# Performance work log

Measured on AMD Instinct MI355X. Metric: run time of the kernel, lower is better.

## Reference

```python
import jax, jax.numpy as jnp
import numpy as np

B, H, N, D = 2, 16, 2048, 64

def setup_inputs() -> dict:
    key = jax.random.key(0)
    ks = jax.random.split(key, 5)
    q = jax.random.normal(ks[0], (B, H, N, D), dtype=jnp.float32)
    k = jax.random.normal(ks[1], (B, H, N, D), dtype=jnp.float32)
    v = jax.random.normal(ks[2], (B, H, N, D), dtype=jnp.float32)
    # 1x1 Conv2d(heads, heads, bias=False) == HxH linear mixing over the head dim
    W_pre = jax.random.normal(ks[3], (H, H), dtype=jnp.float32) * (1.0 / jnp.sqrt(H))
    W_post = jax.random.normal(ks[4], (H, H), dtype=jnp.float32) * (1.0 / jnp.sqrt(H))
    return {"q": q, "k": k, "v": v, "W_pre": W_pre, "W_post": W_post}

def reference(q, k, v, W_pre, W_post):
    heads = q.shape[1]
    d_head = q.shape[-1]
    # original: scale = (1/sqrt(heads)) / sqrt(d_head)
    scale = 1.0 / (jnp.sqrt(jnp.float32(heads)) * jnp.sqrt(jnp.float32(d_head)))
    # pre-softmax talking heads applied to BOTH q and k (head-mixing linear)
    q = jnp.einsum('ef,bfnd->bend', W_pre, q)
    k = jnp.einsum('ef,bfnd->bend', W_pre, k)
    attn_weights = jnp.einsum('bhid,bhjd->bhij', q, k) * scale  # [B,H,N,N]
    i = q.shape[-2]
    j = k.shape[-2]
    causal_mask = jnp.triu(jnp.ones((i, j), dtype=bool), k=1)
    attn_weights = jnp.where(causal_mask, -jnp.inf, attn_weights)
    # softmax computed in float32 (dtype=torch.float32 in attn_fn)
    attn_probs = jax.nn.softmax(attn_weights.astype(jnp.float32), axis=-1)
    # dropout p=0.0 -> identity
    attn_probs = jnp.einsum('ef,bfij->beij', W_post, attn_probs)
    attn_output = jnp.einsum('bhij,bhjd->bhid', attn_probs, v)
    return attn_output
```

## Files before the change

kernel.cpp:

```cpp
#include <hip/hip_runtime.h>
#include <math.h>

typedef _Float16 Hh;
typedef __attribute__((ext_vector_type(8))) _Float16 half8;
typedef __attribute__((ext_vector_type(4))) _Float16 half4;
typedef __attribute__((ext_vector_type(4))) float float4v;

#define B_ 2
#define H_ 16
#define N_ 2048
#define D_ 64
#define ND_ (N_*D_)
#define C1 0.04508422f

#define BAR() asm volatile("s_waitcnt lgkmcnt(0)\n\ts_barrier" ::: "memory")

#define EB_JS 324
#define EB_IS 20
#define PM_ES 580
#define PM_IS 36

__global__ __launch_bounds__(256) void prep_kernel(const float* __restrict__ q,
    const float* __restrict__ k, const float* __restrict__ v,
    const float* __restrict__ Wpre,
    Hh* __restrict__ qb, Hh* __restrict__ kb, Hh* __restrict__ vt2,
    float4* __restrict__ out4, float4* __restrict__ lacc4)
{
    int tid = threadIdx.x;
    int bid = blockIdx.x;
    if (bid < 512) {
        __shared__ float wsh[256];
        wsh[tid] = Wpre[tid];
        __syncthreads();
        int tensor = bid >> 8;
        int g = ((bid & 255) << 8) | tid;
        int b = g >> 15;
        int r = g & 32767;
        const float4* src = (const float4*)(tensor ? k : q);
        Hh* dst = tensor ? kb : qb;
        float4 x[16];
        #pragma unroll
        for (int f=0; f<16; f++) x[f] = src[(size_t)(b*16+f)*32768 + r];
        #pragma unroll
        for (int e=0; e<16; e++) {
            float4 a = make_float4(0.f,0.f,0.f,0.f);
            #pragma unroll
            for (int f=0; f<16; f++) {
                float wv = wsh[e*16+f];
                a.x += wv*x[f].x; a.y += wv*x[f].y; a.z += wv*x[f].z; a.w += wv*x[f].w;
            }
            half4 hv; hv[0]=(Hh)a.x; hv[1]=(Hh)a.y; hv[2]=(Hh)a.z; hv[3]=(Hh)a.w;
            *(half4*)(dst + (size_t)(b*16+e)*ND_ + (size_t)r*4) = hv;
        }
    } else if (bid < 768) {
        __shared__ Hh tile[64*48];
        int tb = bid - 512;
        int be = tb >> 3;
        int jtg = tb & 7;
        const float4* v4 = (const float4*)v;
        for (int u=0; u<8; u++) {
            int jt = jtg*8 + u;
            #pragma unroll
            for (int p=0; p<2; p++) {
                int j = p*16 + (tid>>4);
                int d4 = tid & 15;
                float4 val = v4[(size_t)be*32768 + (size_t)(jt*32+j)*16 + d4];
                tile[(d4*4+0)*48 + j] = (Hh)val.x;
                tile[(d4*4+1)*48 + j] = (Hh)val.y;
                tile[(d4*4+2)*48 + j] = (Hh)val.z;
                tile[(d4*4+3)*48 + j] = (Hh)val.w;
            }
            BAR();
            {
                int d = tid >> 2;
                int jc = (tid & 3) * 8;
                half8 o;
                #pragma unroll
                for (int z=0; z<8; z++) o[z] = tile[d*48 + jc + z];
                *(half8*)(vt2 + ((size_t)(be*64) + jt)*2048 + (size_t)tid*8) = o;
            }
            BAR();
        }
    } else {
        int zid = (bid - 768) * 256 + tid;
        float4 zz = make_float4(0.f,0.f,0.f,0.f);
        #pragma unroll
        for (int u=0; u<4; u++) out4[(size_t)u*262144 + zid] = zz;
        if (zid < 16384) lacc4[zid] = zz;
    }
}

__global__ __launch_bounds__(1024,4) void denom_kernel(const Hh* __restrict__ qb,
    const Hh* __restrict__ kb, float* __restrict__ lacc_g)
{
    int bid = blockIdx.x;
    int s = bid & 7;
    int idx = bid >> 3;
    int b = idx & 1;
    int pr = idx >> 1;
    int tid = threadIdx.x;
    int lane = tid & 63, w = tid >> 6;
    int qd = lane >> 4, c = lane & 15;

    const Hh* qh = qb + (size_t)(b*16 + w)*ND_;
    const Hh* kh = kb + (size_t)(b*16 + w)*ND_;

    for (int half = 0; half < 2; half++) {
        int it = half ? (31 - pr) : pr;
        int i0 = it * 64;

        half8 aq[4][2];
        #pragma unroll
        for (int ig=0; ig<4; ig++) {
            const Hh* qr = qh + (size_t)(i0 + ig*16 + c)*64 + qd*8;
            aq[ig][0] = *(const half8*)qr;
            aq[ig][1] = *(const half8*)(qr+32);
        }
        float lacc[4][4];
        #pragma unroll
        for (int ig=0; ig<4; ig++)
            #pragma unroll
            for (int r=0; r<4; r++) lacc[ig][r] = 0.f;

        int jtmax = 2*it + 1;
        for (int jt = s; jt <= jtmax; jt += 8) {
            int j0 = jt*32;
            #pragma unroll
            for (int jh=0; jh<2; jh++) {
                const Hh* kr = kh + (size_t)(j0 + jh*16 + c)*64 + qd*8;
                half8 b0 = *(const half8*)kr;
                half8 b1 = *(const half8*)(kr+32);
                int j = j0 + jh*16 + c;
                #pragma unroll
                for (int ig=0; ig<4; ig++) {
                    float4v sv = {0.f,0.f,0.f,0.f};
                    sv = __builtin_amdgcn_mfma_f32_16x16x32_f16(aq[ig][0], b0, sv, 0,0,0);
                    sv = __builtin_amdgcn_mfma_f32_16x16x32_f16(aq[ig][1], b1, sv, 0,0,0);
                    #pragma unroll
                    for (int r=0; r<4; r++) {
                        int i = i0 + ig*16 + qd*4 + r;
                        float ev = (j <= i) ? __builtin_amdgcn_exp2f(sv[r]*C1) : 0.f;
                        lacc[ig][r] += ev;
                    }
                }
            }
        }
        #pragma unroll
        for (int ig=0; ig<4; ig++) {
            #pragma unroll
            for (int r=0; r<4; r++) {
                float vs = lacc[ig][r];
                vs += __shfl_xor(vs, 1);
                vs += __shfl_xor(vs, 2);
                vs += __shfl_xor(vs, 4);
                vs += __shfl_xor(vs, 8);
                if (c == 0)
                    unsafeAtomicAdd(&lacc_g[(size_t)(b*16+w)*N_ + i0 + ig*16 + qd*4 + r], vs);
            }
        }
    }
}

__global__ __launch_bounds__(512,4) void attend_kernel(const Hh* __restrict__ qb,
    const Hh* __restrict__ kb, const Hh* __restrict__ vt2,
    const float* __restrict__ lacc_g, const float* __restrict__ Wpost,
    float* __restrict__ out)
{
    __shared__ Hh Ebuf[32*EB_JS];
    __shared__ Hh Pm[16*PM_ES];

    int bid = blockIdx.x;
    int s = (bid & 7) >> 1;
    int idxp = ((bid >> 3) << 1) | (bid & 1);
    int idx = 255 - idxp;
    int b = idx & 1, it = idx >> 1;
    int jtmax = it >> 1;
    if (s > jtmax) return;
    int i0 = it * 16;

    int tid = threadIdx.x;
    int lane = tid & 63, w = tid >> 6;
    int qd = lane >> 4, c = lane & 15;

    int fg = w & 3, jh = w >> 2;
    half8 aq[4][2];
    float lgr[4][4];
    #pragma unroll
    for (int ff=0; ff<4; ff++) {
        int f = 4*fg + ff;
        const Hh* qr = qb + (size_t)((b*16+f)*N_ + i0 + c)*64 + qd*8;
        aq[ff][0] = *(const half8*)qr;
        aq[ff][1] = *(const half8*)(qr+32);
        #pragma unroll
        for (int r=0; r<4; r++)
            lgr[ff][r] = __builtin_amdgcn_logf(
                lacc_g[(size_t)(b*16+f)*N_ + i0 + qd*4 + r]);
    }
    int jh2 = w & 1, ib = 4*(w>>1);
    half4 wf;
    #pragma unroll
    for (int z=0; z<4; z++) wf[z] = (Hh)Wpost[c*16 + qd*4 + z];

    float4v acc[2][4];
    #pragma unroll
    for (int el=0; el<2; el++) for (int nc=0; nc<4; nc++)
        acc[el][nc] = (float4v){0.f,0.f,0.f,0.f};

    auto scores = [&](int jt) {
        int jc = jt*32 + jh*16;
        float4v sv[4];
        #pragma unroll
        for (int ff=0; ff<4; ff++) {
            int f = 4*fg + ff;
            const Hh* kr = kb + (size_t)((b*16+f)*N_ + jc + c)*64 + qd*8;
            half8 b0 = *(const half8*)kr;
            half8 b1 = *(const half8*)(kr+32);
            float4v t = {0.f,0.f,0.f,0.f};
            t = __builtin_amdgcn_mfma_f32_16x16x32_f16(aq[ff][0], b0, t, 0,0,0);
            t = __builtin_amdgcn_mfma_f32_16x16x32_f16(aq[ff][1], b1, t, 0,0,0);
            sv[ff] = t;
        }
        int j = jc + c;
        #pragma unroll
        for (int r=0; r<4; r++) {
            int i = i0 + qd*4 + r;
            half4 h;
            #pragma unroll
            for (int ff=0; ff<4; ff++)
                h[ff] = (Hh)((j <= i) ? __builtin_amdgcn_exp2f(sv[ff][r]*C1 - lgr[ff][r]) : 0.f);
            *(half4*)&Ebuf[(jh*16+c)*EB_JS + (qd*4+r)*EB_IS + fg*4] = h;
        }
    };

    scores(s);
    BAR();

    for (int jt = s; jt <= jtmax; jt += 4) {
        #pragma unroll
        for (int ii=0; ii<4; ii++) {
            int i = ib + ii;
            half4 ef = *(const half4*)&Ebuf[(jh2*16+c)*EB_JS + i*EB_IS + qd*4];
            float4v cc = {0.f,0.f,0.f,0.f};
            cc = __builtin_amdgcn_mfma_f32_16x16x16f16(ef, wf, cc, 0,0,0);
            half4 hv;
            #pragma unroll
            for (int r=0; r<4; r++) hv[r] = (Hh)cc[r];
            *(half4*)&Pm[c*PM_ES + i*PM_IS + jh2*16 + qd*4] = hv;
        }
        BAR();
        #pragma unroll
        for (int el=0; el<2; el++) {
            int e = 2*w + el;
            half8 pa = *(const half8*)&Pm[e*PM_ES + c*PM_IS + qd*8];
            #pragma unroll
            for (int nc=0; nc<4; nc++) {
                const Hh* vr = vt2 + (size_t)((b*16+e)*64 + jt)*2048 + (nc*16+c)*32 + qd*8;
                half8 vb = *(const half8*)vr;
                acc[el][nc] = __builtin_amdgcn_mfma_f32_16x16x32_f16(pa, vb, acc[el][nc], 0,0,0);
            }
        }
        if (jt + 4 <= jtmax) scores(jt + 4);
        BAR();
    }

    #pragma unroll
    for (int el=0; el<2; el++) {
        int e = 2*w + el;
        #pragma unroll
        for (int nc0=0; nc0<4; nc0++) {
            int nc = (nc0 + s) & 3;
            #pragma unroll
            for (int r=0; r<4; r++)
                unsafeAtomicAdd(&out[(size_t)((b*16+e)*N_ + i0 + qd*4 + r)*64 + nc*16 + c],
                                acc[el][nc][r]);
        }
    }
}

extern "C" void kernel_launch(void* const* d_in, const int* in_sizes, int n_in,
                              void* d_out, int out_size, void* d_ws, size_t ws_size,
                              hipStream_t stream) {
    const float* q     = (const float*)d_in[0];
    const float* k     = (const float*)d_in[1];
    const float* v     = (const float*)d_in[2];
    const float* Wpre  = (const float*)d_in[3];
    const float* Wpost = (const float*)d_in[4];
    float* out = (float*)d_out;

    size_t tsz = (size_t)B_*H_*N_*D_;
    Hh* qb = (Hh*)d_ws;
    Hh* kb = qb + tsz;
    Hh* vt2 = kb + tsz;
    float* lacc = (float*)(vt2 + tsz);

    prep_kernel<<<1792, 256, 0, stream>>>(q, k, v, Wpre, qb, kb, vt2,
                                          (float4*)out, (float4*)lacc);
    denom_kernel<<<256, 1024, 0, stream>>>(qb, kb, lacc);
    attend_kernel<<<1024, 512, 0, stream>>>(qb, kb, vt2, lacc, Wpost, out);
}
```

Before: 249.0 us.

## Double attend query tile to 32 rows and pair light/heavy causal tiles per block

The attend kernel now processes 32-row query tiles with 1024-thread blocks. Each K and V load is shared by twice as many query rows, and the LDS score and probability buffers are widened to match. Each block handles two tiles, pr and 63-pr, back to back so the causal work per block is even, and the grid shrinks from 1024 to 256 blocks. The cost is fewer, larger blocks: roughly one block per CU with bigger LDS use, which may reduce latency hiding.

```diff
diff --git a/kernel.cpp b/kernel.cpp
--- a/kernel.cpp
+++ b/kernel.cpp
@@ -15,9 +15,9 @@
 
 #define BAR() asm volatile("s_waitcnt lgkmcnt(0)\n\ts_barrier" ::: "memory")
 
-#define EB_JS 324
+#define EB_JS 644
 #define EB_IS 20
-#define PM_ES 580
+#define PM_ES 1156
 #define PM_IS 36
 
 __global__ __launch_bounds__(256) void prep_kernel(const float* __restrict__ q,
@@ -161,7 +161,7 @@
     }
 }
 
-__global__ __launch_bounds__(512,4) void attend_kernel(const Hh* __restrict__ qb,
+__global__ __launch_bounds__(1024,4) void attend_kernel(const Hh* __restrict__ qb,
     const Hh* __restrict__ kb, const Hh* __restrict__ vt2,
     const float* __restrict__ lacc_g, const float* __restrict__ Wpost,
     float* __restrict__ out)
@@ -171,108 +171,109 @@
 
     int bid = blockIdx.x;
     int s = (bid & 7) >> 1;
-    int idxp = ((bid >> 3) << 1) | (bid & 1);
-    int idx = 255 - idxp;
-    int b = idx & 1, it = idx >> 1;
-    int jtmax = it >> 1;
-    if (s > jtmax) return;
-    int i0 = it * 16;
+    int idx = ((bid >> 3) << 1) | (bid & 1);
+    int b = idx & 1, pr = idx >> 1;
 
     int tid = threadIdx.x;
     int lane = tid & 63, w = tid >> 6;
     int qd = lane >> 4, c = lane & 15;
 
-    int fg = w & 3, jh = w >> 2;
-    half8 aq[4][2];
-    float lgr[4][4];
-    #pragma unroll
-    for (int ff=0; ff<4; ff++) {
-        int f = 4*fg + ff;
-        const Hh* qr = qb + (size_t)((b*16+f)*N_ + i0 + c)*64 + qd*8;
-        aq[ff][0] = *(const half8*)qr;
-        aq[ff][1] = *(const half8*)(qr+32);
-        #pragma unroll
-        for (int r=0; r<4; r++)
-            lgr[ff][r] = __builtin_amdgcn_logf(
-                lacc_g[(size_t)(b*16+f)*N_ + i0 + qd*4 + r]);
-    }
-    int jh2 = w & 1, ib = 4*(w>>1);
+    int fg = w & 3, jh = (w >> 2) & 1, ig = w >> 3;
+    int jh2 = w & 1, ib = 4*(w >> 1);
     half4 wf;
     #pragma unroll
     for (int z=0; z<4; z++) wf[z] = (Hh)Wpost[c*16 + qd*4 + z];
 
-    float4v acc[2][4];
-    #pragma unroll
-    for (int el=0; el<2; el++) for (int nc=0; nc<4; nc++)
-        acc[el][nc] = (float4v){0.f,0.f,0.f,0.f};
-
-    auto scores = [&](int jt) {
-        int jc = jt*32 + jh*16;
-        float4v sv[4];
+    for (int hf = 0; hf < 2; hf++) {
+        int it = hf ? (63 - pr) : pr;
+        if (s > it) continue;
+        int i0 = it * 32;
+
+        half8 aq[4][2];
+        float lgr[4][4];
         #pragma unroll
         for (int ff=0; ff<4; ff++) {
             int f = 4*fg + ff;
-            const Hh* kr = kb + (size_t)((b*16+f)*N_ + jc + c)*64 + qd*8;
-            half8 b0 = *(const half8*)kr;
-            half8 b1 = *(const half8*)(kr+32);
-            float4v t = {0.f,0.f,0.f,0.f};
-            t = __builtin_amdgcn_mfma_f32_16x16x32_f16(aq[ff][0], b0, t, 0,0,0);
-            t = __builtin_amdgcn_mfma_f32_16x16x32_f16(aq[ff][1], b1, t, 0,0,0);
-            sv[ff] = t;
-        }
-        int j = jc + c;
-        #pragma unroll
-        for (int r=0; r<4; r++) {
-            int i = i0 + qd*4 + r;
-            half4 h;
-            #pragma unroll
-            for (int ff=0; ff<4; ff++)
-                h[ff] = (Hh)((j <= i) ? __builtin_amdgcn_exp2f(sv[ff][r]*C1 - lgr[ff][r]) : 0.f);
-            *(half4*)&Ebuf[(jh*16+c)*EB_JS + (qd*4+r)*EB_IS + fg*4] = h;
-        }
-    };
-
-    scores(s);
-    BAR();
-
-    for (int jt = s; jt <= jtmax; jt += 4) {
-        #pragma unroll
-        for (int ii=0; ii<4; ii++) {
-            int i = ib + ii;
-            half4 ef = *(const half4*)&Ebuf[(jh2*16+c)*EB_JS + i*EB_IS + qd*4];
-            float4v cc = {0.f,0.f,0.f,0.f};
-            cc = __builtin_amdgcn_mfma_f32_16x16x16f16(ef, wf, cc, 0,0,0);
-            half4 hv;
-            #pragma unroll
-            for (int r=0; r<4; r++) hv[r] = (Hh)cc[r];
-            *(half4*)&Pm[c*PM_ES + i*PM_IS + jh2*16 + qd*4] = hv;
-        }
+            const Hh* qr = qb + (size_t)((b*16+f)*N_ + i0 + ig*16 + c)*64 + qd*8;
+            aq[ff][0] = *(const half8*)qr;
+            aq[ff][1] = *(const half8*)(qr+32);
+            #pragma unroll
+            for (int r=0; r<4; r++)
+                lgr[ff][r] = __builtin_amdgcn_logf(
+                    lacc_g[(size_t)(b*16+f)*N_ + i0 + ig*16 + qd*4 + r]);
+        }
+
+        float4v acc[2][4];
+        #pragma unroll
+        for (int ig2=0; ig2<2; ig2++) for (int nc=0; nc<4; nc++)
+            acc[ig2][nc] = (float4v){0.f,0.f,0.f,0.f};
+
+        auto scores = [&](int jt) {
+            int jc = jt*32 + jh*16;
+            float4v sv[4];
+            #pragma unroll
+            for (int ff=0; ff<4; ff++) {
+                int f = 4*fg + ff;
+                const Hh* kr = kb + (size_t)((b*16+f)*N_ + jc + c)*64 + qd*8;
+                half8 b0 = *(const half8*)kr;
+                half8 b1 = *(const half8*)(kr+32);
+                float4v t = {0.f,0.f,0.f,0.f};
+                t = __builtin_amdgcn_mfma_f32_16x16x32_f16(aq[ff][0], b0, t, 0,0,0);
+                t = __builtin_amdgcn_mfma_f32_16x16x32_f16(aq[ff][1], b1, t, 0,0,0);
+                sv[ff] = t;
+            }
+            int j = jc + c;
+            #pragma unroll
+            for (int r=0; r<4; r++) {
+                int i = i0 + ig*16 + qd*4 + r;
+                half4 h;
+                #pragma unroll
+                for (int ff=0; ff<4; ff++)
+                    h[ff] = (Hh)((j <= i) ? __builtin_amdgcn_exp2f(sv[ff][r]*C1 - lgr[ff][r]) : 0.f);
+                *(half4*)&Ebuf[(jh*16+c)*EB_JS + (ig*16 + qd*4 + r)*EB_IS + fg*4] = h;
+            }
+        };
+
+        scores(s);
         BAR();
-        #pragma unroll
-        for (int el=0; el<2; el++) {
-            int e = 2*w + el;
-            half8 pa = *(const half8*)&Pm[e*PM_ES + c*PM_IS + qd*8];
-            #pragma unroll
-            for (int nc=0; nc<4; nc++) {
-                const Hh* vr = vt2 + (size_t)((b*16+e)*64 + jt)*2048 + (nc*16+c)*32 + qd*8;
-                half8 vb = *(const half8*)vr;
-                acc[el][nc] = __builtin_amdgcn_mfma_f32_16x16x32_f16(pa, vb, acc[el][nc], 0,0,0);
-            }
-        }
-        if (jt + 4 <= jtmax) scores(jt + 4);
-        BAR();
-    }
-
-    #pragma unroll
-    for (int el=0; el<2; el++) {
-        int e = 2*w + el;
-        #pragma unroll
-        for (int nc0=0; nc0<4; nc0++) {
-            int nc = (nc0 + s) & 3;
-            #pragma unroll
-            for (int r=0; r<4; r++)
-                unsafeAtomicAdd(&out[(size_t)((b*16+e)*N_ + i0 + qd*4 + r)*64 + nc*16 + c],
-                                acc[el][nc][r]);
+
+        for (int jt = s; jt <= it; jt += 4) {
+            #pragma unroll
+            for (int ii=0; ii<4; ii++) {
+                int i = ib + ii;
+                half4 ef = *(const half4*)&Ebuf[(jh2*16+c)*EB_JS + i*EB_IS + qd*4];
+                float4v cc = {0.f,0.f,0.f,0.f};
+                cc = __builtin_amdgcn_mfma_f32_16x16x16f16(ef, wf, cc, 0,0,0);
+                half4 hv;
+                #pragma unroll
+                for (int r=0; r<4; r++) hv[r] = (Hh)cc[r];
+                *(half4*)&Pm[c*PM_ES + i*PM_IS + jh2*16 + qd*4] = hv;
+            }
+            BAR();
+            #pragma unroll
+            for (int ig2=0; ig2<2; ig2++) {
+                half8 pa = *(const half8*)&Pm[w*PM_ES + (ig2*16 + c)*PM_IS + qd*8];
+                #pragma unroll
+                for (int nc=0; nc<4; nc++) {
+                    const Hh* vr = vt2 + (size_t)((b*16+w)*64 + jt)*2048 + (nc*16+c)*32 + qd*8;
+                    half8 vb = *(const half8*)vr;
+                    acc[ig2][nc] = __builtin_amdgcn_mfma_f32_16x16x32_f16(pa, vb, acc[ig2][nc], 0,0,0);
+                }
+            }
+            if (jt + 4 <= it) scores(jt + 4);
+            BAR();
+        }
+
+        #pragma unroll
+        for (int ig2=0; ig2<2; ig2++) {
+            #pragma unroll
+            for (int nc0=0; nc0<4; nc0++) {
+                int nc = (nc0 + s) & 3;
+                #pragma unroll
+                for (int r=0; r<4; r++)
+                    unsafeAtomicAdd(&out[(size_t)((b*16+w)*N_ + i0 + ig2*16 + qd*4 + r)*64 + nc*16 + c],
+                                    acc[ig2][nc][r]);
+            }
         }
     }
 }
@@ -296,5 +297,5 @@
     prep_kernel<<<1792, 256, 0, stream>>>(q, k, v, Wpre, qb, kb, vt2,
                                           (float4*)out, (float4*)lacc);
     denom_kernel<<<256, 1024, 0, stream>>>(qb, kb, lacc);
-    attend_kernel<<<1024, 512, 0, stream>>>(qb, kb, vt2, lacc, Wpost, out);
+    attend_kernel<<<256, 1024, 0, stream>>>(qb, kb, vt2, lacc, Wpost, out);
 }
```

Measured after the change: 252.6 us. Within noise of the previous version (+1.5%).

## Prefetch K tiles, split denom heads across blocks, pair attend row tiles

Applied to the files above, without the earlier changes.

The denominator kernel now launches 1024 blocks of 256 threads, each covering four heads instead of sixteen. Its inner loop double-buffers K fragments in registers so the next tile's loads are in flight while the current tile's MFMAs run. The attend kernel prefetches the next K tile into registers before the head-mixing and PV stage, and each block now handles a balanced pair of row tiles (pr and 127-pr) so causal work per block is even, with half as many blocks. The extra register buffers and the lowered occupancy hints may reduce occupancy or cause spills.

```diff
diff --git a/kernel.cpp b/kernel.cpp
--- a/kernel.cpp
+++ b/kernel.cpp
@@ -20,7 +20,7 @@
 #define PM_ES 580
 #define PM_IS 36
 
-__global__ __launch_bounds__(256) void prep_kernel(const float* __restrict__ q,
+__global__ void prep_kernel(const float* __restrict__ q,
     const float* __restrict__ k, const float* __restrict__ v,
     const float* __restrict__ Wpre,
     Hh* __restrict__ qb, Hh* __restrict__ kb, Hh* __restrict__ vt2,
@@ -90,23 +90,26 @@
     }
 }
 
-__global__ __launch_bounds__(1024,4) void denom_kernel(const Hh* __restrict__ qb,
+__global__ __launch_bounds__(256,1)
+void denom_kernel(const Hh* __restrict__ qb,
     const Hh* __restrict__ kb, float* __restrict__ lacc_g)
 {
     int bid = blockIdx.x;
     int s = bid & 7;
-    int idx = bid >> 3;
+    int hg = (bid >> 3) & 3;
+    int idx = bid >> 5;
     int b = idx & 1;
     int pr = idx >> 1;
     int tid = threadIdx.x;
     int lane = tid & 63, w = tid >> 6;
+    int f = hg*4 + w;
     int qd = lane >> 4, c = lane & 15;
 
-    const Hh* qh = qb + (size_t)(b*16 + w)*ND_;
-    const Hh* kh = kb + (size_t)(b*16 + w)*ND_;
-
-    for (int half = 0; half < 2; half++) {
-        int it = half ? (31 - pr) : pr;
+    const Hh* qh = qb + (size_t)(b*16 + f)*ND_;
+    const Hh* kh = kb + (size_t)(b*16 + f)*ND_;
+
+    for (int hf = 0; hf < 2; hf++) {
+        int it = hf ? (31 - pr) : pr;
         int i0 = it * 64;
 
         half8 aq[4][2];
@@ -122,20 +125,23 @@
             #pragma unroll
             for (int r=0; r<4; r++) lacc[ig][r] = 0.f;
 
-        int jtmax = 2*it + 1;
-        for (int jt = s; jt <= jtmax; jt += 8) {
-            int j0 = jt*32;
+        auto loadK = [&](int jt, half8 (&kk)[2][2]) {
             #pragma unroll
             for (int jh=0; jh<2; jh++) {
-                const Hh* kr = kh + (size_t)(j0 + jh*16 + c)*64 + qd*8;
-                half8 b0 = *(const half8*)kr;
-                half8 b1 = *(const half8*)(kr+32);
-                int j = j0 + jh*16 + c;
+                const Hh* kr = kh + (size_t)(jt*32 + jh*16 + c)*64 + qd*8;
+                kk[jh][0] = *(const half8*)kr;
+                kk[jh][1] = *(const half8*)(kr+32);
+            }
+        };
+        auto compute = [&](int jt, half8 (&kk)[2][2]) {
+            #pragma unroll
+            for (int jh=0; jh<2; jh++) {
+                int j = jt*32 + jh*16 + c;
                 #pragma unroll
                 for (int ig=0; ig<4; ig++) {
                     float4v sv = {0.f,0.f,0.f,0.f};
-                    sv = __builtin_amdgcn_mfma_f32_16x16x32_f16(aq[ig][0], b0, sv, 0,0,0);
-                    sv = __builtin_amdgcn_mfma_f32_16x16x32_f16(aq[ig][1], b1, sv, 0,0,0);
+                    sv = __builtin_amdgcn_mfma_f32_16x16x32_f16(aq[ig][0], kk[jh][0], sv, 0,0,0);
+                    sv = __builtin_amdgcn_mfma_f32_16x16x32_f16(aq[ig][1], kk[jh][1], sv, 0,0,0);
                     #pragma unroll
                     for (int r=0; r<4; r++) {
                         int i = i0 + ig*16 + qd*4 + r;
@@ -144,6 +150,19 @@
                     }
                 }
             }
+        };
+
+        int jtmax = 2*it + 1;
+        half8 ka[2][2], kn[2][2];
+        loadK(s, ka);
+        for (int jt = s; jt <= jtmax; jt += 16) {
+            bool m1 = (jt + 8 <= jtmax);
+            if (m1) loadK(jt + 8, kn);
+            compute(jt, ka);
+            if (m1) {
+                if (jt + 16 <= jtmax) loadK(jt + 16, ka);
+                compute(jt + 8, kn);
+            }
         }
         #pragma unroll
         for (int ig=0; ig<4; ig++) {
@@ -155,13 +174,14 @@
                 vs += __shfl_xor(vs, 4);
                 vs += __shfl_xor(vs, 8);
                 if (c == 0)
-                    unsafeAtomicAdd(&lacc_g[(size_t)(b*16+w)*N_ + i0 + ig*16 + qd*4 + r], vs);
+                    unsafeAtomicAdd(&lacc_g[(size_t)(b*16+f)*N_ + i0 + ig*16 + qd*4 + r], vs);
             }
         }
     }
 }
 
-__global__ __launch_bounds__(512,4) void attend_kernel(const Hh* __restrict__ qb,
+__global__ __launch_bounds__(512,2)
+void attend_kernel(const Hh* __restrict__ qb,
     const Hh* __restrict__ kb, const Hh* __restrict__ vt2,
     const float* __restrict__ lacc_g, const float* __restrict__ Wpost,
     float* __restrict__ out)
@@ -171,108 +191,123 @@
 
     int bid = blockIdx.x;
     int s = (bid & 7) >> 1;
-    int idxp = ((bid >> 3) << 1) | (bid & 1);
-    int idx = 255 - idxp;
-    int b = idx & 1, it = idx >> 1;
-    int jtmax = it >> 1;
-    if (s > jtmax) return;
-    int i0 = it * 16;
+    int idx = ((bid >> 3) << 1) | (bid & 1);
+    int b = idx & 1;
+    int pr = idx >> 1;
 
     int tid = threadIdx.x;
     int lane = tid & 63, w = tid >> 6;
     int qd = lane >> 4, c = lane & 15;
 
     int fg = w & 3, jh = w >> 2;
-    half8 aq[4][2];
-    float lgr[4][4];
-    #pragma unroll
-    for (int ff=0; ff<4; ff++) {
-        int f = 4*fg + ff;
-        const Hh* qr = qb + (size_t)((b*16+f)*N_ + i0 + c)*64 + qd*8;
-        aq[ff][0] = *(const half8*)qr;
-        aq[ff][1] = *(const half8*)(qr+32);
-        #pragma unroll
-        for (int r=0; r<4; r++)
-            lgr[ff][r] = __builtin_amdgcn_logf(
-                lacc_g[(size_t)(b*16+f)*N_ + i0 + qd*4 + r]);
-    }
-    int jh2 = w & 1, ib = 4*(w>>1);
+    int jh2 = w & 1, ib = 4*(w >> 1);
     half4 wf;
     #pragma unroll
     for (int z=0; z<4; z++) wf[z] = (Hh)Wpost[c*16 + qd*4 + z];
 
-    float4v acc[2][4];
-    #pragma unroll
-    for (int el=0; el<2; el++) for (int nc=0; nc<4; nc++)
-        acc[el][nc] = (float4v){0.f,0.f,0.f,0.f};
-
-    auto scores = [&](int jt) {
-        int jc = jt*32 + jh*16;
-        float4v sv[4];
+    for (int hf = 0; hf < 2; hf++) {
+        int it = hf ? (127 - pr) : pr;
+        int jtmax = it >> 1;
+        if (s > jtmax) continue;
+        int i0 = it * 16;
+
+        half8 aq[4][2];
+        float lgr[4][4];
         #pragma unroll
         for (int ff=0; ff<4; ff++) {
             int f = 4*fg + ff;
-            const Hh* kr = kb + (size_t)((b*16+f)*N_ + jc + c)*64 + qd*8;
-            half8 b0 = *(const half8*)kr;
-            half8 b1 = *(const half8*)(kr+32);
-            float4v t = {0.f,0.f,0.f,0.f};
-            t = __builtin_amdgcn_mfma_f32_16x16x32_f16(aq[ff][0], b0, t, 0,0,0);
-            t = __builtin_amdgcn_mfma_f32_16x16x32_f16(aq[ff][1], b1, t, 0,0,0);
-            sv[ff] = t;
-        }
-        int j = jc + c;
-        #pragma unroll
-        for (int r=0; r<4; r++) {
-            int i = i0 + qd*4 + r;
-            half4 h;
-            #pragma unroll
-            for (int ff=0; ff<4; ff++)
-                h[ff] = (Hh)((j <= i) ? __builtin_amdgcn_exp2f(sv[ff][r]*C1 - lgr[ff][r]) : 0.f);
-            *(half4*)&Ebuf[(jh*16+c)*EB_JS + (qd*4+r)*EB_IS + fg*4] = h;
-        }
-    };
-
-    scores(s);
-    BAR();
-
-    for (int jt = s; jt <= jtmax; jt += 4) {
-        #pragma unroll
-        for (int ii=0; ii<4; ii++) {
-            int i = ib + ii;
-            half4 ef = *(const half4*)&Ebuf[(jh2*16+c)*EB_JS + i*EB_IS + qd*4];
-            float4v cc = {0.f,0.f,0.f,0.f};
-            cc = __builtin_amdgcn_mfma_f32_16x16x16f16(ef, wf, cc, 0,0,0);
-            half4 hv;
-            #pragma unroll
-            for (int r=0; r<4; r++) hv[r] = (Hh)cc[r];
-            *(half4*)&Pm[c*PM_ES + i*PM_IS + jh2*16 + qd*4] = hv;
-        }
+            const Hh* qr = qb + (size_t)((b*16+f)*N_ + i0 + c)*64 + qd*8;
+            aq[ff][0] = *(const half8*)qr;
+            aq[ff][1] = *(const half8*)(qr+32);
+            #pragma unroll
+            for (int r=0; r<4; r++)
+                lgr[ff][r] = __builtin_amdgcn_logf(
+                    lacc_g[(size_t)(b*16+f)*N_ + i0 + qd*4 + r]);
+        }
+
+        float4v acc[2][4];
+        #pragma unroll
+        for (int el=0; el<2; el++) for (int nc=0; nc<4; nc++)
+            acc[el][nc] = (float4v){0.f,0.f,0.f,0.f};
+
+        auto loadK = [&](int jt, half8 (&kk)[4][2]) {
+            int jc = jt*32 + jh*16;
+            #pragma unroll
+            for (int ff=0; ff<4; ff++) {
+                int f = 4*fg + ff;
+                const Hh* kr = kb + (size_t)((b*16+f)*N_ + jc + c)*64 + qd*8;
+                kk[ff][0] = *(const half8*)kr;
+                kk[ff][1] = *(const half8*)(kr+32);
+            }
+        };
+        auto scores = [&](int jt, half8 (&kk)[4][2]) {
+            int j = jt*32 + jh*16 + c;
+            float4v sv[4];
+            #pragma unroll
+            for (int ff=0; ff<4; ff++) {
+                float4v t = {0.f,0.f,0.f,0.f};
+                t = __builtin_amdgcn_mfma_f32_16x16x32_f16(aq[ff][0], kk[ff][0], t, 0,0,0);
+                t = __builtin_amdgcn_mfma_f32_16x16x32_f16(aq[ff][1], kk[ff][1], t, 0,0,0);
+                sv[ff] = t;
+            }
+            #pragma unroll
+            for (int r=0; r<4; r++) {
+                int i = i0 + qd*4 + r;
+                half4 h;
+                #pragma unroll
+                for (int ff=0; ff<4; ff++)
+                    h[ff] = (Hh)((j <= i) ?
+                        __builtin_amdgcn_exp2f(sv[ff][r]*C1 - lgr[ff][r]) : 0.f);
+                *(half4*)&Ebuf[(jh*16+c)*EB_JS + (qd*4+r)*EB_IS + fg*4] = h;
+            }
+        };
+
+        half8 kn[4][2];
+        loadK(s, kn);
+        scores(s, kn);
         BAR();
+
+        for (int jt = s; jt <= jtmax; jt += 4) {
+            bool more = (jt + 4 <= jtmax);
+            if (more) loadK(jt + 4, kn);
+            #pragma unroll
+            for (int ii=0; ii<4; ii++) {
+                int i = ib + ii;
+                half4 ef = *(const half4*)&Ebuf[(jh2*16+c)*EB_JS + i*EB_IS + qd*4];
+                float4v cc = {0.f,0.f,0.f,0.f};
+                cc = __builtin_amdgcn_mfma_f32_16x16x16f16(ef, wf, cc, 0,0,0);
+                half4 hv;
+                #pragma unroll
+                for (int r=0; r<4; r++) hv[r] = (Hh)cc[r];
+                *(half4*)&Pm[c*PM_ES + i*PM_IS + jh2*16 + qd*4] = hv;
+            }
+            BAR();
+            #pragma unroll
+            for (int el=0; el<2; el++) {
+                int e = 2*w + el;
+                half8 pa = *(const half8*)&Pm[e*PM_ES + c*PM_IS + qd*8];
+                #pragma unroll
+                for (int nc=0; nc<4; nc++) {
+                    const Hh* vr = vt2 + (size_t)((b*16+e)*64 + jt)*2048 + (nc*16+c)*32 + qd*8;
+                    half8 vb = *(const half8*)vr;
+                    acc[el][nc] = __builtin_amdgcn_mfma_f32_16x16x32_f16(pa, vb, acc[el][nc], 0,0,0);
+                }
+            }
+            if (more) scores(jt + 4, kn);
+            BAR();
+        }
+
         #pragma unroll
         for (int el=0; el<2; el++) {
             int e = 2*w + el;
-            half8 pa = *(const half8*)&Pm[e*PM_ES + c*PM_IS + qd*8];
-            #pragma unroll
-            for (int nc=0; nc<4; nc++) {
-                const Hh* vr = vt2 + (size_t)((b*16+e)*64 + jt)*2048 + (nc*16+c)*32 + qd*8;
-                half8 vb = *(const half8*)vr;
-                acc[el][nc] = __builtin_amdgcn_mfma_f32_16x16x32_f16(pa, vb, acc[el][nc], 0,0,0);
-            }
-        }
-        if (jt + 4 <= jtmax) scores(jt + 4);
-        BAR();
-    }
-
-    #pragma unroll
-    for (int el=0; el<2; el++) {
-        int e = 2*w + el;
-        #pragma unroll
-        for (int nc0=0; nc0<4; nc0++) {
-            int nc = (nc0 + s) & 3;
-            #pragma unroll
-            for (int r=0; r<4; r++)
-                unsafeAtomicAdd(&out[(size_t)((b*16+e)*N_ + i0 + qd*4 + r)*64 + nc*16 + c],
-                                acc[el][nc][r]);
+            #pragma unroll
+            for (int nc0=0; nc0<4; nc0++) {
+                int nc = (nc0 + s) & 3;
+                #pragma unroll
+                for (int r=0; r<4; r++)
+                    unsafeAtomicAdd(&out[(size_t)((b*16+e)*N_ + i0 + qd*4 + r)*64 + nc*16 + c],
+                                    acc[el][nc][r]);
+            }
         }
     }
 }
@@ -295,6 +330,6 @@
 
     prep_kernel<<<1792, 256, 0, stream>>>(q, k, v, Wpre, qb, kb, vt2,
                                           (float4*)out, (float4*)lacc);
-    denom_kernel<<<256, 1024, 0, stream>>>(qb, kb, lacc);
-    attend_kernel<<<1024, 512, 0, stream>>>(qb, kb, vt2, lacc, Wpost, out);
+    denom_kernel<<<1024, 256, 0, stream>>>(qb, kb, lacc);
+    attend_kernel<<<512, 512, 0, stream>>>(qb, kb, vt2, lacc, Wpost, out);
 }
```

Result: slower. 268.0 us (+7.6%).
